# Kernel tuning notes

Measured on AMD Instinct MI355X. Metric: run time of the kernel, lower is better.

## Reference

```python
import jax, jax.numpy as jnp
from jax import lax
import numpy as np

GRID, IMG, BLOCK = 60, 960, 16
BN_EPS = 1e-5


def _conv(x, w, b):
    return lax.conv_general_dilated(x, w, (1, 1), 'SAME', dimension_numbers=('NCHW', 'OIHW', 'NCHW')) + b[None, :, None, None]


def _bn(x, g, b):
    # inference BatchNorm with running_mean=0, running_var=1
    s = g * np.float32(1.0 / np.sqrt(1.0 + BN_EPS))
    return x * s[None, :, None, None] + b[None, :, None, None]


def _mlp(x, w1, b1, w2, b2):
    return jax.nn.relu(x @ w1.T + b1) @ w2.T + b2


def _lstm_layer(x, wih, whh, b):
    # x: [B,T,D]; torch gate order i,f,g,o; zero initial state
    B = x.shape[0]
    H = whh.shape[1]
    pre = jnp.swapaxes(x, 0, 1) @ wih.T + b  # [T,B,4H]

    def step(carry, p):
        h, c = carry
        z = p + h @ whh.T
        i, f, g, o = jnp.split(z, 4, axis=-1)
        c = jax.nn.sigmoid(f) * c + jax.nn.sigmoid(i) * jnp.tanh(g)
        h = jax.nn.sigmoid(o) * jnp.tanh(c)
        return (h, c), h

    z0 = jnp.zeros((B, H), x.dtype)
    (h, c), ys = lax.scan(step, (z0, z0), pre)
    return jnp.swapaxes(ys, 0, 1), h, c


def _forward(motion_vectors, boxes, track_ids, conv1_w, conv1_b, bn1_g, bn1_b, conv2_w, conv2_b, bn2_g, bn2_b, conv3_w, conv3_b, bn3_g, bn3_b, agg_w1, agg_b1, agg_w2, agg_b2, bx_w1, bx_b1, bx_w2, bx_b2, id_table, proj_w, proj_b, empty_slot, l0_wih, l0_whh, l0_b, l1_wih, l1_whh, l1_b, hb_w1, hb_b1, hb_w2, hb_b2, hc_w1, hc_b1, hc_w2, hc_b2, ht_w1, ht_b1, ht_w2, ht_b2):
    B = motion_vectors.shape[0]
    # ---- grid encoder (Conv-BN-ReLU x3) ----
    x = jax.nn.relu(_bn(_conv(motion_vectors, conv1_w, conv1_b), bn1_g, bn1_b))
    x = jax.nn.relu(_bn(_conv(x, conv2_w, conv2_b), bn2_g, bn2_b))
    gf = jax.nn.relu(_bn(_conv(x, conv3_w, conv3_b), bn3_g, bn3_b))  # [B,64,60,60]
    global_feat = gf.mean((-2, -1))  # AdaptiveAvgPool2d(1) -> [B,64]

    # ---- per-box motion statistics (vectorized masked reductions) ----
    bg = jnp.clip(boxes * (IMG / BLOCK), 0.0, GRID - 1e-6)  # grid coords
    ix1 = jnp.floor(bg[..., 0]); iy1 = jnp.floor(bg[..., 1])
    ix2 = jnp.maximum(ix1 + 1.0, jnp.ceil(bg[..., 2]))
    iy2 = jnp.maximum(iy1 + 1.0, jnp.ceil(bg[..., 3]))
    g = jnp.arange(GRID, dtype=bg.dtype)
    mx_ = (g >= ix1[..., None]) & (g < ix2[..., None])  # [B,N,60]
    my_ = (g >= iy1[..., None]) & (g < iy2[..., None])
    mask = my_[..., :, None] & mx_[..., None, :]  # [B,N,60,60]
    m = mask.astype(bg.dtype)
    cnt = m.sum((-2, -1))[..., None]  # [B,N,1], >= 1 by construction
    mv = motion_vectors  # [B,2,60,60]
    s1 = jnp.einsum('bnyx,bcyx->bnc', m, mv)
    s2 = jnp.einsum('bnyx,bcyx->bnc', m, mv * mv)
    mean = s1 / cnt
    var = (s2 - cnt * mean * mean) / jnp.maximum(cnt - 1.0, 1.0)  # unbiased, like torch .std()
    var_safe = jnp.where(cnt > 1.0, jnp.maximum(var, 1e-12), 1.0)
    std = jnp.where(cnt > 1.0, jnp.sqrt(var_safe), 0.0)
    BIG = jnp.asarray(1e9, bg.dtype)
    mn = jnp.min(jnp.where(mask[:, :, None], mv[:, None], BIG), axis=(-2, -1))   # [B,N,2]
    mx = jnp.max(jnp.where(mask[:, :, None], mv[:, None], -BIG), axis=(-2, -1))  # [B,N,2]
    stats = jnp.stack([mean[..., 0], mean[..., 1], std[..., 0], std[..., 1], mn[..., 0], mx[..., 0], mn[..., 1], mx[..., 1]], -1)  # [B,N,8]
    motion_emb = _mlp(stats, agg_w1, agg_b1, agg_w2, agg_b2)  # [B,N,64]

    # ---- slot initialization ----
    box_emb = _mlp(boxes, bx_w1, bx_b1, bx_w2, bx_b2)  # [B,N,64]
    id_emb = id_table[jnp.clip(track_ids, 0, 999)]  # [B,N,32]
    obj = jnp.concatenate([box_emb, id_emb, motion_emb], -1)  # [B,N,160]
    slots = obj @ proj_w.T + proj_b  # [B,300,128]; N == max_slots so no empty slots used

    # ---- 2-layer LSTM over the 300 slots (batch_first, eval -> no dropout) ----
    Ns = slots.shape[1]
    gexp = jnp.broadcast_to(global_feat[:, None, :], (B, Ns, global_feat.shape[-1]))
    lstm_in = jnp.concatenate([slots, gexp], -1)  # [B,300,192]
    y, h0, c0 = _lstm_layer(lstm_in, l0_wih, l0_whh, l0_b)
    y, h1, c1 = _lstm_layer(y, l1_wih, l1_whh, l1_b)  # [B,300,128]

    # ---- RT-DETR style heads ----
    pred_boxes = jax.nn.sigmoid(_mlp(y, hb_w1, hb_b1, hb_w2, hb_b2))  # [B,300,4]
    cls_logits = _mlp(y, hc_w1, hc_b1, hc_w2, hc_b2)  # [B,300,2]
    tid_logits = _mlp(y, ht_w1, ht_b1, ht_w2, ht_b2)  # [B,300,1000]
    h = jnp.stack([h0, h1])
    c = jnp.stack([c0, c1])
    return pred_boxes, cls_logits, tid_logits, h, c


def setup_inputs() -> dict:
    B, N = 32, 300
    key = jax.random.key(0)
    ks = iter(jax.random.split(key, 60))

    def w(*s):
        return jax.random.normal(next(ks), s, jnp.float32) * 0.05

    mv = jax.random.normal(next(ks), (B, 2, GRID, GRID), jnp.float32)
    bb = jax.random.uniform(next(ks), (B, N, 4), jnp.float32)
    boxes = jnp.concatenate([jnp.minimum(bb[..., :2], bb[..., 2:]), jnp.maximum(bb[..., :2], bb[..., 2:])], -1)
    track_ids = jax.random.randint(next(ks), (B, N), 0, 1000)
    return dict(
        motion_vectors=mv, boxes=boxes, track_ids=track_ids,
        conv1_w=w(32, 2, 3, 3), conv1_b=w(32), bn1_g=1.0 + w(32), bn1_b=w(32),
        conv2_w=w(64, 32, 3, 3), conv2_b=w(64), bn2_g=1.0 + w(64), bn2_b=w(64),
        conv3_w=w(64, 64, 3, 3), conv3_b=w(64), bn3_g=1.0 + w(64), bn3_b=w(64),
        agg_w1=w(32, 8), agg_b1=w(32), agg_w2=w(64, 32), agg_b2=w(64),
        bx_w1=w(32, 4), bx_b1=w(32), bx_w2=w(64, 32), bx_b2=w(64),
        id_table=w(1000, 32).at[0].set(0.0),
        proj_w=w(128, 160), proj_b=w(128), empty_slot=w(128),
        l0_wih=w(512, 192), l0_whh=w(512, 128), l0_b=w(512),
        l1_wih=w(512, 128), l1_whh=w(512, 128), l1_b=w(512),
        hb_w1=w(256, 128), hb_b1=w(256), hb_w2=w(4, 256), hb_b2=w(4),
        hc_w1=w(256, 128), hc_b1=w(256), hc_w2=w(2, 256), hc_b2=w(2),
        ht_w1=w(256, 128), ht_b1=w(256), ht_w2=w(1000, 256), ht_b2=w(1000))


def reference(motion_vectors, boxes, track_ids, conv1_w, conv1_b, bn1_g, bn1_b, conv2_w, conv2_b, bn2_g, bn2_b, conv3_w, conv3_b, bn3_g, bn3_b, agg_w1, agg_b1, agg_w2, agg_b2, bx_w1, bx_b1, bx_w2, bx_b2, id_table, proj_w, proj_b, empty_slot, l0_wih, l0_whh, l0_b, l1_wih, l1_whh, l1_b, hb_w1, hb_b1, hb_w2, hb_b2, hc_w1, hc_b1, hc_w2, hc_b2, ht_w1, ht_b1, ht_w2, ht_b2):
    return _forward(motion_vectors, boxes, track_ids, conv1_w, conv1_b, bn1_g, bn1_b, conv2_w, conv2_b, bn2_g, bn2_b, conv3_w, conv3_b, bn3_g, bn3_b, agg_w1, agg_b1, agg_w2, agg_b2, bx_w1, bx_b1, bx_w2, bx_b2, id_table, proj_w, proj_b, empty_slot, l0_wih, l0_whh, l0_b, l1_wih, l1_whh, l1_b, hb_w1, hb_b1, hb_w2, hb_b2, hc_w1, hc_b1, hc_w2, hc_b2, ht_w1, ht_b1, ht_w2, ht_b2)
```

## Files before the change

kernel.cpp:

```cpp
#include <hip/hip_runtime.h>
#include <hip/hip_bf16.h>
#include <math.h>

typedef unsigned short ushort_t;
typedef __attribute__((ext_vector_type(8))) short bf16x8;
typedef __attribute__((ext_vector_type(4))) float f32x4;

#define LOG2E 1.4426950408889634f

__device__ __forceinline__ float sigf(float x) {
  x = fminf(fmaxf(x, -30.f), 30.f);
  return 1.f / (1.f + __expf(-x));
}
__device__ __forceinline__ ushort_t f2bf(float x) {
  unsigned int b = __float_as_uint(x);
  unsigned int lsb = (b >> 16) & 1u;
  b += 0x7fffu + lsb;
  return (ushort_t)(b >> 16);
}
__device__ __forceinline__ float bf2f(ushort_t u) {
  return __uint_as_float(((unsigned int)u) << 16);
}
__device__ __forceinline__ float gsc(int g3) {
  return (g3 == 2) ? (2.f * LOG2E) : LOG2E;
}

#define NPIX 3600
__device__ __forceinline__ int gperm(int rho) {
  return ((rho & 3) << 7) + (rho >> 2);
}

__global__ __launch_bounds__(256) void gvec_kernel(
    const float* __restrict__ wih0, const float* __restrict__ gf,
    float* __restrict__ gvec) {
  int i = blockIdx.x * 256 + threadIdx.x;
  int b = i >> 9, n = i & 511;
  const float* wr = wih0 + gperm(n) * 192 + 128;
  const float* g = gf + b * 64;
  float a = 0.f;
#pragma unroll
  for (int k = 0; k < 64; ++k) a = fmaf(wr[k], g[k], a);
  gvec[i] = a * (1.f / 3600.f) * gsc(n & 3);
}

__global__ __launch_bounds__(256) void front_kernel(
    const float* __restrict__ mv, const float* __restrict__ c1w,
    const float* __restrict__ c1b, const float* __restrict__ bg1,
    const float* __restrict__ bb1, ushort_t* __restrict__ x1out,
    const float* __restrict__ boxes, const int* __restrict__ ids,
    const float* __restrict__ agg_w1, const float* __restrict__ agg_b1,
    const float* __restrict__ agg_w2, const float* __restrict__ agg_b2,
    const float* __restrict__ bx_w1, const float* __restrict__ bx_b1,
    const float* __restrict__ bx_w2, const float* __restrict__ bx_b2,
    const float* __restrict__ id_table, ushort_t* __restrict__ obj_out,
    const float* __restrict__ conv2_w, const float* __restrict__ conv3_w,
    const float* __restrict__ wih0, const float* __restrict__ projW,
    const float* __restrict__ projb, const float* __restrict__ l0_b,
    const float* __restrict__ hbw1, const float* __restrict__ hcw1,
    const float* __restrict__ htw1, const float* __restrict__ htw2,
    const float* __restrict__ hbb1, const float* __restrict__ hcb1,
    const float* __restrict__ htb1, ushort_t* __restrict__ wc2,
    ushort_t* __restrict__ wc3, ushort_t* __restrict__ wAp,
    float* __restrict__ l0bp, ushort_t* __restrict__ whid,
    ushort_t* __restrict__ wt2, float* __restrict__ bhid) {
  if (blockIdx.x < 1989) {
    int i = blockIdx.x * 256 + threadIdx.x;
    if (i < 18432) {
      int oc = i / 288, r = i % 288, kt = r / 32, ic = r % 32;
      wc2[i] = f2bf(conv2_w[((oc * 32 + ic) * 3 + kt / 3) * 3 + kt % 3]);
      return;
    }
    i -= 18432;
    if (i < 36864) {
      int oc = i / 576, r = i % 576, c = r / 288, r2 = r % 288;
      int kt = r2 / 32, icl = r2 % 32, ic = c * 32 + icl;
      wc3[i] = f2bf(conv3_w[((oc * 64 + ic) * 3 + kt / 3) * 3 + kt % 3]);
      return;
    }
    i -= 36864;
    if (i < 98304) {
      int n = i / 192, k = i % 192;
      int src = gperm(n);
      float a = 0.f;
      if (k < 160) {
        const float* wr = wih0 + src * 192;
        for (int j = 0; j < 128; ++j) a = fmaf(wr[j], projW[j * 160 + k], a);
      }
      wAp[i] = f2bf(a * gsc(n & 3));
      return;
    }
    i -= 98304;
    if (i < 512) {
      int src = gperm(i);
      float a = l0_b[src];
      const float* wr = wih0 + src * 192;
      for (int j = 0; j < 128; ++j) a = fmaf(wr[j], projb[j], a);
      l0bp[i] = a * gsc(i & 3);
      return;
    }
    i -= 512;
    if (i < 98304) {
      int row = i >> 7, c = i & 127;
      float v = (row < 256)   ? hbw1[row * 128 + c]
                : (row < 512) ? hcw1[(row - 256) * 128 + c]
                              : htw1[(row - 512) * 128 + c];
      whid[i] = f2bf(v);
      return;
    }
    i -= 98304;
    if (i < 256000) {
      wt2[i] = f2bf(htw2[i]);
      return;
    }
    i -= 256000;
    if (i < 768)
      bhid[i] = (i < 256) ? hbb1[i] : (i < 512) ? hcb1[i - 256] : htb1[i - 512];
    return;
  }
  int bx = blockIdx.x - 1989;
  if (bx < 14400) {
    int idx = bx * 256 + threadIdx.x;
    int x = idx % 60;
    int y = (idx / 60) % 60;
    int oc = (idx / 3600) % 32;
    int b = idx / (3600 * 32);
    float acc = 0.f;
#pragma unroll
    for (int ic = 0; ic < 2; ++ic) {
      const float* src = mv + (b * 2 + ic) * NPIX;
      const float* wp = c1w + (oc * 2 + ic) * 9;
#pragma unroll
      for (int ky = 0; ky < 3; ++ky) {
        int gy = y + ky - 1;
        if (gy < 0 || gy >= 60) continue;
#pragma unroll
        for (int kx = 0; kx < 3; ++kx) {
          int gx = x + kx - 1;
          if (gx < 0 || gx >= 60) continue;
          acc = fmaf(src[gy * 60 + gx], wp[ky * 3 + kx], acc);
        }
      }
    }
    float s = bg1[oc] * rsqrtf(1.f + 1e-5f);
    float v = fmaf(acc, s, fmaf(c1b[oc], s, bb1[oc]));
    x1out[idx] = f2bf(fmaxf(v, 0.f));
    return;
  }
  __shared__ float obj[2][160];
  __shared__ float hm[2][32];
  __shared__ float hbx[2][32];
  __shared__ float stats[2][8];
  __shared__ float boxf[2][4];
  __shared__ float red[2][2][8];
  int h = threadIdx.x >> 7;
  int t = threadIdx.x & 127;
  int blk = (bx - 14400) * 2 + h;
  int b = blk / 300;
  float bx0 = boxes[blk * 4 + 0], by0 = boxes[blk * 4 + 1];
  float bx1 = boxes[blk * 4 + 2], by1 = boxes[blk * 4 + 3];
  const float HI = (float)(60.0 - 1e-6);
  float gx1 = fminf(fmaxf(bx0 * 60.f, 0.f), HI);
  float gy1 = fminf(fmaxf(by0 * 60.f, 0.f), HI);
  float gx2 = fminf(fmaxf(bx1 * 60.f, 0.f), HI);
  float gy2 = fminf(fmaxf(by1 * 60.f, 0.f), HI);
  float fx1 = floorf(gx1), fy1 = floorf(gy1);
  float fx2 = fmaxf(fx1 + 1.f, ceilf(gx2));
  float fy2 = fmaxf(fy1 + 1.f, ceilf(gy2));
  int ix1 = (int)fx1, iy1 = (int)fy1, ix2 = (int)fx2, iy2 = (int)fy2;
  int w = ix2 - ix1, hgt = iy2 - iy1;
  int area = w * hgt;
  float s0 = 0.f, s1 = 0.f, q0 = 0.f, q1 = 0.f;
  float mn0 = 1e9f, mn1 = 1e9f, mx0 = -1e9f, mx1 = -1e9f;
  const float* mv0 = mv + b * 2 * NPIX;
  const float* mv1 = mv0 + NPIX;
  for (int i = t; i < area; i += 128) {
    int r = i / w, cc = i - r * w;
    int yy = iy1 + r, xx = ix1 + cc;
    float v0 = mv0[yy * 60 + xx];
    float v1 = mv1[yy * 60 + xx];
    s0 += v0; q0 += v0 * v0; mn0 = fminf(mn0, v0); mx0 = fmaxf(mx0, v0);
    s1 += v1; q1 += v1 * v1; mn1 = fminf(mn1, v1); mx1 = fmaxf(mx1, v1);
  }
#pragma unroll
  for (int off = 32; off; off >>= 1) {
    s0 += __shfl_down(s0, off); s1 += __shfl_down(s1, off);
    q0 += __shfl_down(q0, off); q1 += __shfl_down(q1, off);
    mn0 = fminf(mn0, __shfl_down(mn0, off));
    mn1 = fminf(mn1, __shfl_down(mn1, off));
    mx0 = fmaxf(mx0, __shfl_down(mx0, off));
    mx1 = fmaxf(mx1, __shfl_down(mx1, off));
  }
  if ((t & 63) == 0) {
    int wv = t >> 6;
    red[h][wv][0] = s0; red[h][wv][1] = s1;
    red[h][wv][2] = q0; red[h][wv][3] = q1;
    red[h][wv][4] = mn0; red[h][wv][5] = mn1;
    red[h][wv][6] = mx0; red[h][wv][7] = mx1;
  }
  __syncthreads();
  if (t == 0) {
    float S0 = red[h][0][0] + red[h][1][0], S1 = red[h][0][1] + red[h][1][1];
    float Q0 = red[h][0][2] + red[h][1][2], Q1 = red[h][0][3] + red[h][1][3];
    float MN0 = fminf(red[h][0][4], red[h][1][4]);
    float MN1 = fminf(red[h][0][5], red[h][1][5]);
    float MX0 = fmaxf(red[h][0][6], red[h][1][6]);
    float MX1 = fmaxf(red[h][0][7], red[h][1][7]);
    float cnt = (float)area;
    float mean0 = S0 / cnt, mean1 = S1 / cnt;
    float var0 = (Q0 - cnt * mean0 * mean0) / fmaxf(cnt - 1.f, 1.f);
    float var1 = (Q1 - cnt * mean1 * mean1) / fmaxf(cnt - 1.f, 1.f);
    float sd0 = (cnt > 1.f) ? sqrtf(fmaxf(var0, 1e-12f)) : 0.f;
    float sd1 = (cnt > 1.f) ? sqrtf(fmaxf(var1, 1e-12f)) : 0.f;
    stats[h][0] = mean0; stats[h][1] = mean1; stats[h][2] = sd0;
    stats[h][3] = sd1; stats[h][4] = MN0; stats[h][5] = MX0;
    stats[h][6] = MN1; stats[h][7] = MX1;
    boxf[h][0] = bx0; boxf[h][1] = by0; boxf[h][2] = bx1; boxf[h][3] = by1;
  }
  __syncthreads();
  if (t < 32) {
    float a = agg_b1[t];
#pragma unroll
    for (int k = 0; k < 8; ++k) a = fmaf(stats[h][k], agg_w1[t * 8 + k], a);
    hm[h][t] = fmaxf(a, 0.f);
  } else if (t < 64) {
    int j = t - 32;
    float a = bx_b1[j];
#pragma unroll
    for (int k = 0; k < 4; ++k) a = fmaf(boxf[h][k], bx_w1[j * 4 + k], a);
    hbx[h][j] = fmaxf(a, 0.f);
  }
  __syncthreads();
  if (t < 64) {
    float a = bx_b2[t];
#pragma unroll
    for (int k = 0; k < 32; ++k) a = fmaf(hbx[h][k], bx_w2[t * 32 + k], a);
    obj[h][t] = a;
  } else {
    int j = t - 64;
    float a = agg_b2[j];
#pragma unroll
    for (int k = 0; k < 32; ++k) a = fmaf(hm[h][k], agg_w2[j * 32 + k], a);
    obj[h][96 + j] = a;
  }
  if (t < 32) {
    int id = ids[blk];
    id = min(max(id, 0), 999);
    obj[h][64 + t] = id_table[id * 32 + t];
  }
  __syncthreads();
  obj_out[(size_t)blk * 192 + t] = f2bf(obj[h][t]);
  if (t < 32) {
    obj_out[(size_t)blk * 192 + 128 + t] = f2bf(obj[h][128 + t]);
    obj_out[(size_t)blk * 192 + 160 + t] = 0;
  }
}

template <int CIN, bool POOL>
__global__ __launch_bounds__(256) void conv_mfma_kernel(
    const ushort_t* __restrict__ in, const ushort_t* __restrict__ wc,
    const float* __restrict__ cb, const float* __restrict__ bg,
    const float* __restrict__ bb, ushort_t* __restrict__ out,
    float* __restrict__ gf) {
  constexpr int NCHUNK = CIN / 32;
  __shared__ ushort_t in_lds[18 * 18 * 40];
  int tid = threadIdx.x;
  int wv = tid >> 6, lane = tid & 63;
  int col = lane & 15, kg = lane >> 4;
  int b = blockIdx.y, tile = blockIdx.x;
  int tq = tile >> 2, tr = tile & 3;
  int ty0 = tq * 16 - (tq == 3 ? 4 : 0);
  int tx0 = tr * 16 - (tr == 3 ? 4 : 0);
  int oc = wv * 16 + col;

  bf16x8 bw[NCHUNK * 9];
#pragma unroll
  for (int c = 0; c < NCHUNK; ++c)
#pragma unroll
    for (int kt = 0; kt < 9; ++kt)
      bw[c * 9 + kt] = *(const bf16x8*)(wc + oc * (NCHUNK * 288) + c * 288 +
                                        kt * 32 + kg * 8);

  f32x4 acc[16];
#pragma unroll
  for (int m = 0; m < 16; ++m) acc[m] = (f32x4){0.f, 0.f, 0.f, 0.f};

  for (int c = 0; c < NCHUNK; ++c) {
    if (c) __syncthreads();
    for (int i = tid; i < 18 * 18 * 32; i += 256) {
      int ic = i / 324, rem = i % 324;
      int yy = rem / 18, xx = rem % 18;
      int gy = ty0 + yy - 1, gx = tx0 + xx - 1;
      ushort_t v = 0;
      if (gy >= 0 && gy < 60 && gx >= 0 && gx < 60)
        v = in[((size_t)(b * CIN + c * 32 + ic) * 60 + gy) * 60 + gx];
      in_lds[(yy * 18 + xx) * 40 + ic] = v;
    }
    __syncthreads();
#pragma unroll
    for (int kt = 0; kt < 9; ++kt) {
      int ky = kt / 3, kx = kt % 3;
#pragma unroll
      for (int m = 0; m < 16; ++m) {
        bf16x8 af =
            *(const bf16x8*)(&in_lds[((m + ky) * 18 + col + kx) * 40 + kg * 8]);
        acc[m] = __builtin_amdgcn_mfma_f32_16x16x32_bf16(af, bw[c * 9 + kt],
                                                         acc[m], 0, 0, 0);
      }
    }
  }
  float s = bg[oc] * rsqrtf(1.f + 1e-5f);
  float bias = fmaf(cb[oc], s, bb[oc]);
  float pool = 0.f;
#pragma unroll
  for (int m = 0; m < 16; ++m) {
    float vv[4];
#pragma unroll
    for (int r = 0; r < 4; ++r) vv[r] = fmaxf(fmaf(acc[m][r], s, bias), 0.f);
    if (POOL) {
      bool ymask = (tq != 3) || (m >= 4);
#pragma unroll
      for (int r = 0; r < 4; ++r) {
        int px = kg * 4 + r;
        bool xmask = (tr != 3) || (px >= 4);
        if (ymask && xmask) pool += vv[r];
      }
    } else {
      ushort_t st[4];
#pragma unroll
      for (int r = 0; r < 4; ++r) st[r] = f2bf(vv[r]);
      int yy = ty0 + m, xx = tx0 + kg * 4;
      *(uint2*)(&out[((size_t)(b * 64 + oc) * 60 + yy) * 60 + xx]) =
          *(uint2*)st;
    }
  }
  if (POOL) {
    pool += __shfl_xor(pool, 16);
    pool += __shfl_xor(pool, 32);
    if (lane < 16) atomicAdd(&gf[b * 64 + oc], pool);
  }
}

template <int ACT, bool OBF16, bool GVEC>
__global__ __launch_bounds__(256) void gemm_bf16w_kernel(
    const ushort_t* __restrict__ A, int lda, const ushort_t* __restrict__ W,
    const float* __restrict__ bias, void* __restrict__ C, int ldc, int M,
    int N, int K, const float* __restrict__ gvec) {
  __shared__ ushort_t As[128 * 64];
  __shared__ ushort_t Ws[64 * 64];
  int tid = threadIdx.x;
  int wv = tid >> 6, lane = tid & 63;
  int col = lane & 15, kg = lane >> 4;
  int wm = wv >> 1, wn = wv & 1;
  int m0 = blockIdx.x * 128, n0 = blockIdx.y * 64;
  f32x4 acc[4][2];
#pragma unroll
  for (int i = 0; i < 4; ++i)
#pragma unroll
    for (int j = 0; j < 2; ++j) acc[i][j] = (f32x4){0.f, 0.f, 0.f, 0.f};

  int nk = K >> 6;
  for (int kc = 0; kc < nk; ++kc) {
    if (kc) __syncthreads();
#pragma unroll
    for (int q = 0; q < 4; ++q) {
      int idx = q * 256 + tid;
      int row = idx >> 3, ch = idx & 7;
      uint4 v =
          *(const uint4*)(A + (size_t)(m0 + row) * lda + kc * 64 + ch * 8);
      *(uint4*)(&As[row * 64 + ((ch * 8) ^ ((row & 7) << 3))]) = v;
    }
#pragma unroll
    for (int q = 0; q < 2; ++q) {
      int idx = q * 256 + tid;
      int row = idx >> 3, ch = idx & 7;
      int n = n0 + row;
      uint4 v = make_uint4(0, 0, 0, 0);
      if (n < N) v = *(const uint4*)(W + (size_t)n * K + kc * 64 + ch * 8);
      *(uint4*)(&Ws[row * 64 + ((ch * 8) ^ ((row & 7) << 3))]) = v;
    }
    __syncthreads();
#pragma unroll
    for (int ks = 0; ks < 2; ++ks) {
      bf16x8 bfr[2], afr[4];
#pragma unroll
      for (int ni = 0; ni < 2; ++ni) {
        int row = wn * 32 + ni * 16 + col;
        bfr[ni] = *(const bf16x8*)(
            &Ws[row * 64 + ((ks * 32 + kg * 8) ^ ((row & 7) << 3))]);
      }
#pragma unroll
      for (int mi = 0; mi < 4; ++mi) {
        int row = wm * 64 + mi * 16 + col;
        afr[mi] = *(const bf16x8*)(
            &As[row * 64 + ((ks * 32 + kg * 8) ^ ((row & 7) << 3))]);
      }
#pragma unroll
      for (int mi = 0; mi < 4; ++mi)
#pragma unroll
        for (int ni = 0; ni < 2; ++ni)
          acc[mi][ni] = __builtin_amdgcn_mfma_f32_16x16x32_bf16(
              afr[mi], bfr[ni], acc[mi][ni], 0, 0, 0);
    }
  }
#pragma unroll
  for (int ni = 0; ni < 2; ++ni) {
    int n = n0 + wn * 32 + ni * 16 + col;
    float bn = (n < N) ? bias[n] : 0.f;
#pragma unroll
    for (int mi = 0; mi < 4; ++mi) {
      int mbase = m0 + wm * 64 + mi * 16 + kg * 4;
#pragma unroll
      for (int r = 0; r < 4; ++r) {
        float v = acc[mi][ni][r] + bn;
        if (GVEC) v += gvec[((mbase + r) / 300) * 512 + n];
        if (ACT == 1) v = fmaxf(v, 0.f);
        if (n < N) {
          if (OBF16)
            ((ushort_t*)C)[(size_t)(mbase + r) * ldc + n] = f2bf(v);
          else
            ((float*)C)[(size_t)(mbase + r) * ldc + n] = v;
        }
      }
    }
  }
}

__global__ __launch_bounds__(256) void head_small_kernel(
    const ushort_t* __restrict__ hid, const float* __restrict__ wb2,
    const float* __restrict__ bb2, const float* __restrict__ wc2,
    const float* __restrict__ bc2, float* __restrict__ outB,
    float* __restrict__ outC) {
  int idx = blockIdx.x * 256 + threadIdx.x;
  int row = idx / 6, j = idx % 6;
  const ushort_t* h = hid + (size_t)row * 768 + (j < 4 ? 0 : 256);
  const float* wrow = (j < 4) ? wb2 + j * 256 : wc2 + (j - 4) * 256;
  float acc = (j < 4) ? bb2[j] : bc2[j - 4];
  for (int k = 0; k < 256; k += 8) {
    uint4 hv = *(const uint4*)(h + k);
    unsigned int ww[4] = {hv.x, hv.y, hv.z, hv.w};
#pragma unroll
    for (int q = 0; q < 4; ++q) {
      acc = fmaf(bf2f((ushort_t)(ww[q] & 0xffff)), wrow[k + 2 * q], acc);
      acc = fmaf(bf2f((ushort_t)(ww[q] >> 16)), wrow[k + 2 * q + 1], acc);
    }
  }
  float v = (j < 4) ? sigf(acc) : acc;
  if (j < 4) outB[row * 4 + j] = v;
  else outC[row * 2 + (j - 4)] = v;
}

#define LSTM_BAR() asm volatile("s_waitcnt lgkmcnt(0)\n\ts_barrier" ::: "memory")

__global__ __launch_bounds__(512) void lstm_fused_kernel(
    const float* __restrict__ pre0,
    const float* __restrict__ whh0,
    const float* __restrict__ wih1,
    const float* __restrict__ whh1,
    const float* __restrict__ b1,
    float* __restrict__ pre1,
    ushort_t* __restrict__ y0,
    ushort_t* __restrict__ y1,
    float* __restrict__ outH, float* __restrict__ outC,
    unsigned int* __restrict__ flags)
{
  __shared__ ushort_t h_lds[2][4][160];
  int tid = threadIdx.x;
  int w = tid >> 6, lane = tid & 63;
  int col = lane & 15, kg = lane >> 4;
  int bat = col & 3, q = col >> 2;
  int cell = (4 * w + q) * 4 + kg;
  float wsc = gsc(col & 3);

  if (blockIdx.x < 8) {
    int g = blockIdx.x;
    int b0 = g * 4;
    unsigned int* flagp = &flags[g * 32];
    for (int i = tid; i < 2 * 4 * 160; i += 512) ((ushort_t*)h_lds)[i] = 0;
    bf16x8 aW0[4][4];
#pragma unroll
    for (int j = 0; j < 4; ++j) {
      int rho = (4 * w + j) * 16 + col;
      int src = gperm(rho);
#pragma unroll
      for (int kt = 0; kt < 4; ++kt) {
        const float* s1 = whh0 + src * 128 + kt * 32 + kg * 8;
        bf16x8 f1;
#pragma unroll
        for (int qq = 0; qq < 8; ++qq) f1[qq] = (short)f2bf(s1[qq] * wsc);
        aW0[j][kt] = f1;
      }
    }
    const float* pg = pre0 + (size_t)(b0 + bat) * 300 * 512 + 4 * cell;
    ushort_t* yg0 = y0 + ((size_t)(b0 + bat) * 300) * 128 + cell;
    float c = 0.f, hout = 0.f;
    f32x4 p0v = *(const f32x4*)(pg);
    f32x4 p1v = *(const f32x4*)(pg + 512);
    __syncthreads();

    for (int s = 0; s < 300; ++s) {
      const ushort_t* hb = h_lds[s & 1][bat];
      bf16x8 bfr[4];
#pragma unroll
      for (int kt = 0; kt < 4; ++kt)
        bfr[kt] = *(const bf16x8*)(hb + kt * 32 + kg * 8);
      f32x4 a0 = {0.f, 0.f, 0.f, 0.f}, a1 = a0, a2 = a0, a3 = a0;
#pragma unroll
      for (int kt = 0; kt < 4; ++kt) {
        a0 = __builtin_amdgcn_mfma_f32_16x16x32_bf16(aW0[0][kt], bfr[kt], a0, 0, 0, 0);
        a1 = __builtin_amdgcn_mfma_f32_16x16x32_bf16(aW0[1][kt], bfr[kt], a1, 0, 0, 0);
        a2 = __builtin_amdgcn_mfma_f32_16x16x32_bf16(aW0[2][kt], bfr[kt], a2, 0, 0, 0);
        a3 = __builtin_amdgcn_mfma_f32_16x16x32_bf16(aW0[3][kt], bfr[kt], a3, 0, 0, 0);
      }
      f32x4 z = a0;
      if (q == 1) z = a1;
      if (q == 2) z = a2;
      if (q == 3) z = a3;
      {
        float zi = z[0] + p0v[0];
        float zf = z[1] + p0v[1];
        float zg = z[2] + p0v[2];
        float zo = z[3] + p0v[3];
        float vi = __builtin_amdgcn_rcpf(1.f + __builtin_amdgcn_exp2f(-zi));
        float vf = __builtin_amdgcn_rcpf(1.f + __builtin_amdgcn_exp2f(-zf));
        float vg = 1.f - 2.f * __builtin_amdgcn_rcpf(
                              __builtin_amdgcn_exp2f(zg) + 1.f);
        float vo = __builtin_amdgcn_rcpf(1.f + __builtin_amdgcn_exp2f(-zo));
        c = vf * c + vi * vg;
        hout = vo * (1.f - 2.f * __builtin_amdgcn_rcpf(
                             __builtin_amdgcn_exp2f(2.f * LOG2E * c) + 1.f));
        ushort_t hv = f2bf(hout);
        h_lds[(s + 1) & 1][bat][cell] = hv;
        __builtin_nontemporal_store(hv, yg0 + (size_t)s * 128);
        p0v = p1v;
        int sn = (s + 2 < 300) ? s + 2 : 299;
        p1v = *(const f32x4*)(pg + (size_t)sn * 512);
      }
      asm volatile("s_waitcnt vmcnt(6)" ::: "memory");
      LSTM_BAR();
      if (tid == 0 && s >= 3)
        __hip_atomic_store(flagp, (unsigned int)(s - 3), __ATOMIC_RELAXED,
                           __HIP_MEMORY_SCOPE_AGENT);
    }
    asm volatile("s_waitcnt vmcnt(0)" ::: "memory");
    __syncthreads();
    if (tid == 0)
      __hip_atomic_store(flagp, 300u, __ATOMIC_RELAXED,
                         __HIP_MEMORY_SCOPE_AGENT);
    outH[(b0 + bat) * 128 + cell] = hout;
    outC[(b0 + bat) * 128 + cell] = c;
  } else if (blockIdx.x < 16) {
    int g = blockIdx.x - 8;
    int b0 = g * 4;
    unsigned int* flagp = &flags[g * 32 + 16];
    for (int i = tid; i < 2 * 4 * 160; i += 512) ((ushort_t*)h_lds)[i] = 0;
    bf16x8 aW[4][4];
#pragma unroll
    for (int j = 0; j < 4; ++j) {
      int rho = (4 * w + j) * 16 + col;
      int src = gperm(rho);
#pragma unroll
      for (int kt = 0; kt < 4; ++kt) {
        const float* s1 = whh1 + src * 128 + kt * 32 + kg * 8;
        bf16x8 f1;
#pragma unroll
        for (int qq = 0; qq < 8; ++qq) f1[qq] = (short)f2bf(s1[qq] * wsc);
        aW[j][kt] = f1;
      }
    }
    float bi = b1[cell] * LOG2E, bff = b1[128 + cell] * LOG2E;
    float bgg = b1[256 + cell] * (2.f * LOG2E), boo = b1[384 + cell] * LOG2E;
    const float* pg = pre1 + (size_t)(b0 + bat) * 300 * 512 + 4 * cell;
    ushort_t* yg = y1 + (size_t)(b0 + bat) * 300 * 128 + cell;
    float c = 0.f, hout = 0.f;
    unsigned int fc = 0;
    f32x4 p0v, p1v;
    do {
      fc = __hip_atomic_load(flagp, __ATOMIC_RELAXED,
                             __HIP_MEMORY_SCOPE_AGENT);
      if (fc < 1) __builtin_amdgcn_s_sleep(2);
    } while (fc < 1);
    asm volatile("" ::: "memory");
    p0v = __builtin_nontemporal_load((const f32x4*)(pg));
    while (fc < 2) {
      fc = __hip_atomic_load(flagp, __ATOMIC_RELAXED,
                             __HIP_MEMORY_SCOPE_AGENT);
      if (fc < 2) __builtin_amdgcn_s_sleep(2);
    }
    asm volatile("" ::: "memory");
    p1v = __builtin_nontemporal_load((const f32x4*)(pg + 512));
    __syncthreads();

    for (int t = 0; t < 300; ++t) {
      unsigned int fcn = __hip_atomic_load(flagp, __ATOMIC_RELAXED,
                                           __HIP_MEMORY_SCOPE_AGENT);
      const ushort_t* hb = h_lds[t & 1][bat];
      bf16x8 bfr[4];
#pragma unroll
      for (int kt = 0; kt < 4; ++kt)
        bfr[kt] = *(const bf16x8*)(hb + kt * 32 + kg * 8);
      f32x4 a0 = {0.f, 0.f, 0.f, 0.f}, a1 = a0, a2 = a0, a3 = a0;
#pragma unroll
      for (int kt = 0; kt < 4; ++kt) {
        a0 = __builtin_amdgcn_mfma_f32_16x16x32_bf16(aW[0][kt], bfr[kt], a0, 0, 0, 0);
        a1 = __builtin_amdgcn_mfma_f32_16x16x32_bf16(aW[1][kt], bfr[kt], a1, 0, 0, 0);
        a2 = __builtin_amdgcn_mfma_f32_16x16x32_bf16(aW[2][kt], bfr[kt], a2, 0, 0, 0);
        a3 = __builtin_amdgcn_mfma_f32_16x16x32_bf16(aW[3][kt], bfr[kt], a3, 0, 0, 0);
      }
      f32x4 z = a0;
      if (q == 1) z = a1;
      if (q == 2) z = a2;
      if (q == 3) z = a3;
      {
        float zi = z[0] + p0v[0] + bi;
        float zf = z[1] + p0v[1] + bff;
        float zg = z[2] + p0v[2] + bgg;
        float zo = z[3] + p0v[3] + boo;
        float vi = __builtin_amdgcn_rcpf(1.f + __builtin_amdgcn_exp2f(-zi));
        float vf = __builtin_amdgcn_rcpf(1.f + __builtin_amdgcn_exp2f(-zf));
        float vg = 1.f - 2.f * __builtin_amdgcn_rcpf(
                              __builtin_amdgcn_exp2f(zg) + 1.f);
        float vo = __builtin_amdgcn_rcpf(1.f + __builtin_amdgcn_exp2f(-zo));
        c = vf * c + vi * vg;
        hout = vo * (1.f - 2.f * __builtin_amdgcn_rcpf(
                             __builtin_amdgcn_exp2f(2.f * LOG2E * c) + 1.f));
        ushort_t hv = f2bf(hout);
        h_lds[(t + 1) & 1][bat][cell] = hv;
        yg[(size_t)t * 128] = hv;
        p0v = p1v;
        if (t + 2 < 300) {
          unsigned int need = (unsigned int)(t + 3);
          if (fcn > fc) fc = fcn;
          if (fc < need) {
            do {
              fc = __hip_atomic_load(flagp, __ATOMIC_RELAXED,
                                     __HIP_MEMORY_SCOPE_AGENT);
              if (fc < need) __builtin_amdgcn_s_sleep(2);
            } while (fc < need);
            asm volatile("" ::: "memory");
          }
          p1v = __builtin_nontemporal_load(
              (const f32x4*)(pg + (size_t)(t + 2) * 512));
        }
      }
      LSTM_BAR();
    }
    outH[4096 + (b0 + bat) * 128 + cell] = hout;
    outC[4096 + (b0 + bat) * 128 + cell] = c;
  } else {
    int g = blockIdx.x - 16;
    int b0 = g * 4;
    unsigned int* flag0 = &flags[g * 32];
    unsigned int* flag1 = &flags[g * 32 + 16];
    bf16x8 aU[4][4];
#pragma unroll
    for (int j = 0; j < 4; ++j) {
      int rho = (4 * w + j) * 16 + col;
      int src = gperm(rho);
#pragma unroll
      for (int kt = 0; kt < 4; ++kt) {
        const float* s2 = wih1 + src * 128 + kt * 32 + kg * 8;
        bf16x8 f2;
#pragma unroll
        for (int qq = 0; qq < 8; ++qq) f2[qq] = (short)f2bf(s2[qq] * wsc);
        aU[j][kt] = f2;
      }
    }
    int bb = col & 3;
    int ts = col >> 2;
    const ushort_t* yb = y0 + ((size_t)(b0 + bb) * 300) * 128 + kg * 8;
    unsigned int fc = 0;
    for (int t0 = 0; t0 < 300; t0 += 12) {
      unsigned int need = (unsigned int)(t0 + 11);
      while (fc < need) {
        fc = __hip_atomic_load(flag0, __ATOMIC_RELAXED,
                               __HIP_MEMORY_SCOPE_AGENT);
        if (fc < need) __builtin_amdgcn_s_sleep(2);
      }
      asm volatile("" ::: "memory");
      f32x4 acc[4][3];
#pragma unroll
      for (int j = 0; j < 4; ++j)
#pragma unroll
        for (int ct = 0; ct < 3; ++ct) acc[j][ct] = (f32x4){0.f, 0.f, 0.f, 0.f};
#pragma unroll
      for (int ct = 0; ct < 3; ++ct) {
        int t = t0 + ct * 4 + ts;
        bf16x8 bfr[4];
#pragma unroll
        for (int kt = 0; kt < 4; ++kt)
          bfr[kt] = __builtin_nontemporal_load(
              (const bf16x8*)(yb + (size_t)t * 128 + kt * 32));
#pragma unroll
        for (int kt = 0; kt < 4; ++kt) {
          acc[0][ct] = __builtin_amdgcn_mfma_f32_16x16x32_bf16(aU[0][kt], bfr[kt], acc[0][ct], 0, 0, 0);
          acc[1][ct] = __builtin_amdgcn_mfma_f32_16x16x32_bf16(aU[1][kt], bfr[kt], acc[1][ct], 0, 0, 0);
          acc[2][ct] = __builtin_amdgcn_mfma_f32_16x16x32_bf16(aU[2][kt], bfr[kt], acc[2][ct], 0, 0, 0);
          acc[3][ct] = __builtin_amdgcn_mfma_f32_16x16x32_bf16(aU[3][kt], bfr[kt], acc[3][ct], 0, 0, 0);
        }
      }
#pragma unroll
      for (int ct = 0; ct < 3; ++ct) {
        int t = t0 + ct * 4 + ts;
        float* pd = pre1 + ((size_t)(b0 + bb) * 300 + t) * 512 + kg * 4;
#pragma unroll
        for (int j = 0; j < 4; ++j)
          __builtin_nontemporal_store(acc[j][ct],
                                      (f32x4*)(pd + (4 * w + j) * 16));
      }
      asm volatile("s_waitcnt vmcnt(0)" ::: "memory");
      __syncthreads();
      if (tid == 0)
        __hip_atomic_store(flag1, (unsigned int)(t0 + 12), __ATOMIC_RELAXED,
                           __HIP_MEMORY_SCOPE_AGENT);
    }
  }
}

extern "C" void kernel_launch(void* const* d_in, const int* in_sizes, int n_in,
                              void* d_out, int out_size, void* d_ws,
                              size_t ws_size, hipStream_t stream) {
  const float* mv = (const float*)d_in[0];
  const float* boxes = (const float*)d_in[1];
  const int* track_ids = (const int*)d_in[2];
  const float* conv1_w = (const float*)d_in[3];
  const float* conv1_b = (const float*)d_in[4];
  const float* bn1_g = (const float*)d_in[5];
  const float* bn1_b = (const float*)d_in[6];
  const float* conv2_w = (const float*)d_in[7];
  const float* conv2_b = (const float*)d_in[8];
  const float* bn2_g = (const float*)d_in[9];
  const float* bn2_b = (const float*)d_in[10];
  const float* conv3_w = (const float*)d_in[11];
  const float* conv3_b = (const float*)d_in[12];
  const float* bn3_g = (const float*)d_in[13];
  const float* bn3_b = (const float*)d_in[14];
  const float* agg_w1 = (const float*)d_in[15];
  const float* agg_b1 = (const float*)d_in[16];
  const float* agg_w2 = (const float*)d_in[17];
  const float* agg_b2 = (const float*)d_in[18];
  const float* bx_w1 = (const float*)d_in[19];
  const float* bx_b1 = (const float*)d_in[20];
  const float* bx_w2 = (const float*)d_in[21];
  const float* bx_b2 = (const float*)d_in[22];
  const float* id_table = (const float*)d_in[23];
  const float* proj_w = (const float*)d_in[24];
  const float* proj_b = (const float*)d_in[25];
  const float* l0_wih = (const float*)d_in[27];
  const float* l0_whh = (const float*)d_in[28];
  const float* l0_b = (const float*)d_in[29];
  const float* l1_wih = (const float*)d_in[30];
  const float* l1_whh = (const float*)d_in[31];
  const float* l1_b = (const float*)d_in[32];
  const float* hb_w1 = (const float*)d_in[33];
  const float* hb_b1 = (const float*)d_in[34];
  const float* hb_w2 = (const float*)d_in[35];
  const float* hb_b2 = (const float*)d_in[36];
  const float* hc_w1 = (const float*)d_in[37];
  const float* hc_b1 = (const float*)d_in[38];
  const float* hc_w2 = (const float*)d_in[39];
  const float* hc_b2 = (const float*)d_in[40];
  const float* ht_w1 = (const float*)d_in[41];
  const float* ht_b1 = (const float*)d_in[42];
  const float* ht_w2 = (const float*)d_in[43];
  const float* ht_b2 = (const float*)d_in[44];

  char* wsb = (char*)d_ws;
  ushort_t* x1u = (ushort_t*)(wsb + 0);
  ushort_t* x2u = (ushort_t*)(wsb + 7372800);
  float* pre0 = (float*)(wsb + 0);
  ushort_t* hid = (ushort_t*)(wsb + 0);
  ushort_t* y0g = (ushort_t*)(wsb + 19660800);
  float* gf = (float*)(wsb + 22118400);
  ushort_t* obj = (ushort_t*)(wsb + 22126592);
  float* pre1 = (float*)(wsb + 25812992);
  ushort_t* y1b = (ushort_t*)(wsb + 45473792);
  unsigned int* flags = (unsigned int*)(wsb + 47931392);
  ushort_t* wAp = (ushort_t*)(wsb + 47932416);
  ushort_t* whid = (ushort_t*)(wsb + 48129024);
  ushort_t* wt2 = (ushort_t*)(wsb + 48325632);
  float* bhid = (float*)(wsb + 48837632);
  float* l0bp = (float*)(wsb + 48840704);
  float* gvec = (float*)(wsb + 48842752);
  ushort_t* wc2 = (ushort_t*)(wsb + 48908288);
  ushort_t* wc3 = (ushort_t*)(wsb + 48945152);

  float* outB = (float*)d_out;
  float* outC = outB + 38400;
  float* outT = outB + 57600;
  float* outH = outB + 9657600;
  float* outCc = outB + 9665792;

  hipMemsetAsync(gf, 0, 2048 * sizeof(float), stream);
  hipMemsetAsync(flags, 0, 1024, stream);

  front_kernel<<<21189, 256, 0, stream>>>(
      mv, conv1_w, conv1_b, bn1_g, bn1_b, x1u, boxes, track_ids, agg_w1,
      agg_b1, agg_w2, agg_b2, bx_w1, bx_b1, bx_w2, bx_b2, id_table, obj,
      conv2_w, conv3_w, l0_wih, proj_w, proj_b, l0_b, hb_w1, hc_w1, ht_w1,
      ht_w2, hb_b1, hc_b1, ht_b1, wc2, wc3, wAp, l0bp, whid, wt2, bhid);
  conv_mfma_kernel<32, false><<<dim3(16, 32), 256, 0, stream>>>(
      x1u, wc2, conv2_b, bn2_g, bn2_b, x2u, nullptr);
  conv_mfma_kernel<64, true><<<dim3(16, 32), 256, 0, stream>>>(
      x2u, wc3, conv3_b, bn3_g, bn3_b, nullptr, gf);
  gvec_kernel<<<64, 256, 0, stream>>>(l0_wih, gf, gvec);
  gemm_bf16w_kernel<0, false, true><<<dim3(75, 8), 256, 0, stream>>>(
      obj, 192, wAp, l0bp, pre0, 512, 9600, 512, 192, gvec);
  lstm_fused_kernel<<<24, 512, 0, stream>>>(pre0, l0_whh, l1_wih, l1_whh,
                                            l1_b, pre1, y0g, y1b, outH, outCc,
                                            flags);
  gemm_bf16w_kernel<1, true, false><<<dim3(75, 12), 256, 0, stream>>>(
      y1b, 128, whid, bhid, hid, 768, 9600, 768, 128, nullptr);
  head_small_kernel<<<225, 256, 0, stream>>>(hid, hb_w2, hb_b2, hc_w2, hc_b2,
                                             outB, outC);
  gemm_bf16w_kernel<0, false, false><<<dim3(75, 16), 256, 0, stream>>>(
      hid + 512, 768, wt2, ht_b2, outT, 1000, 9600, 1000, 256, nullptr);
}
```

Baseline: 543.4 us.

## Fuse output heads into LSTM kernel as flag-gated consumer blocks overlapping recurrence

The three head kernels (hidden MLP GEMM, box/class small heads, track GEMM) move into extra blocks of the fused LSTM kernel. The layer-1 blocks publish a progress flag every 30 timesteps, and 80 new blocks each wait for their 30-step chunk before computing that chunk's head outputs. Head work can then overlap the serial LSTM recurrence instead of running after it. In exchange, pre0's workspace is reused as the hidden buffer, the layer-1 loop gains periodic full waits and barriers, and correctness depends on enough blocks being co-resident so the spinning consumers do not starve the producers.

```diff
diff --git a/kernel.cpp b/kernel.cpp
--- a/kernel.cpp
+++ b/kernel.cpp
@@ -425,34 +425,10 @@
   }
 }
 
-__global__ __launch_bounds__(256) void head_small_kernel(
-    const ushort_t* __restrict__ hid, const float* __restrict__ wb2,
-    const float* __restrict__ bb2, const float* __restrict__ wc2,
-    const float* __restrict__ bc2, float* __restrict__ outB,
-    float* __restrict__ outC) {
-  int idx = blockIdx.x * 256 + threadIdx.x;
-  int row = idx / 6, j = idx % 6;
-  const ushort_t* h = hid + (size_t)row * 768 + (j < 4 ? 0 : 256);
-  const float* wrow = (j < 4) ? wb2 + j * 256 : wc2 + (j - 4) * 256;
-  float acc = (j < 4) ? bb2[j] : bc2[j - 4];
-  for (int k = 0; k < 256; k += 8) {
-    uint4 hv = *(const uint4*)(h + k);
-    unsigned int ww[4] = {hv.x, hv.y, hv.z, hv.w};
-#pragma unroll
-    for (int q = 0; q < 4; ++q) {
-      acc = fmaf(bf2f((ushort_t)(ww[q] & 0xffff)), wrow[k + 2 * q], acc);
-      acc = fmaf(bf2f((ushort_t)(ww[q] >> 16)), wrow[k + 2 * q + 1], acc);
-    }
-  }
-  float v = (j < 4) ? sigf(acc) : acc;
-  if (j < 4) outB[row * 4 + j] = v;
-  else outC[row * 2 + (j - 4)] = v;
-}
-
 #define LSTM_BAR() asm volatile("s_waitcnt lgkmcnt(0)\n\ts_barrier" ::: "memory")
 
 __global__ __launch_bounds__(512) void lstm_fused_kernel(
-    const float* __restrict__ pre0,
+    const float* pre0,
     const float* __restrict__ whh0,
     const float* __restrict__ wih1,
     const float* __restrict__ whh1,
@@ -461,21 +437,28 @@
     ushort_t* __restrict__ y0,
     ushort_t* __restrict__ y1,
     float* __restrict__ outH, float* __restrict__ outC,
-    unsigned int* __restrict__ flags)
-{
-  __shared__ ushort_t h_lds[2][4][160];
+    unsigned int* __restrict__ flags,
+    ushort_t* hid16,
+    const ushort_t* __restrict__ whid, const ushort_t* __restrict__ wt2,
+    const float* __restrict__ bhid, const float* __restrict__ hbw2,
+    const float* __restrict__ hbb2, const float* __restrict__ hcw2,
+    const float* __restrict__ hcb2, const float* __restrict__ htb2,
+    float* __restrict__ outB, float* __restrict__ outCls,
+    float* __restrict__ outT) {
+  __shared__ ushort_t smem[30720];
   int tid = threadIdx.x;
   int w = tid >> 6, lane = tid & 63;
   int col = lane & 15, kg = lane >> 4;
   int bat = col & 3, q = col >> 2;
   int cell = (4 * w + q) * 4 + kg;
   float wsc = gsc(col & 3);
+  ushort_t (*h_lds)[4][160] = (ushort_t(*)[4][160])smem;
 
   if (blockIdx.x < 8) {
     int g = blockIdx.x;
     int b0 = g * 4;
     unsigned int* flagp = &flags[g * 32];
-    for (int i = tid; i < 2 * 4 * 160; i += 512) ((ushort_t*)h_lds)[i] = 0;
+    for (int i = tid; i < 2 * 4 * 160; i += 512) smem[i] = 0;
     bf16x8 aW0[4][4];
 #pragma unroll
     for (int j = 0; j < 4; ++j) {
@@ -552,7 +535,8 @@
     int g = blockIdx.x - 8;
     int b0 = g * 4;
     unsigned int* flagp = &flags[g * 32 + 16];
-    for (int i = tid; i < 2 * 4 * 160; i += 512) ((ushort_t*)h_lds)[i] = 0;
+    unsigned int* flagy1 = &flags[g * 32 + 17];
+    for (int i = tid; i < 2 * 4 * 160; i += 512) smem[i] = 0;
     bf16x8 aW[4][4];
 #pragma unroll
     for (int j = 0; j < 4; ++j) {
@@ -642,11 +626,18 @@
               (const f32x4*)(pg + (size_t)(t + 2) * 512));
         }
       }
+      if ((t % 30) == 29) {
+        asm volatile("s_waitcnt vmcnt(0)" ::: "memory");
+        __syncthreads();
+        if (tid == 0)
+          __hip_atomic_store(flagy1, (unsigned int)(t + 1), __ATOMIC_RELAXED,
+                             __HIP_MEMORY_SCOPE_AGENT);
+      }
       LSTM_BAR();
     }
     outH[4096 + (b0 + bat) * 128 + cell] = hout;
     outC[4096 + (b0 + bat) * 128 + cell] = c;
-  } else {
+  } else if (blockIdx.x < 24) {
     int g = blockIdx.x - 16;
     int b0 = g * 4;
     unsigned int* flag0 = &flags[g * 32];
@@ -712,6 +703,137 @@
       if (tid == 0)
         __hip_atomic_store(flag1, (unsigned int)(t0 + 12), __ATOMIC_RELAXED,
                            __HIP_MEMORY_SCOPE_AGENT);
+    }
+  } else {
+    int idx2 = blockIdx.x - 24;
+    int g = idx2 & 7, ck = idx2 >> 3;
+    int b0 = g * 4, t0 = ck * 30;
+    unsigned int* flagy = &flags[g * 32 + 17];
+    unsigned int need = (unsigned int)(t0 + 30);
+    unsigned int fc = 0;
+    while (fc < need) {
+      fc = __hip_atomic_load(flagy, __ATOMIC_RELAXED,
+                             __HIP_MEMORY_SCOPE_AGENT);
+      if (fc < need) __builtin_amdgcn_s_sleep(8);
+    }
+    asm volatile("" ::: "memory");
+    int wm = w >> 2, wn = w & 3;
+    int Rt[4][4];
+    bool Vt[4][4];
+#pragma unroll
+    for (int mi = 0; mi < 4; ++mi)
+#pragma unroll
+      for (int r = 0; r < 4; ++r) {
+        int m = wm * 64 + mi * 16 + kg * 4 + r;
+        Vt[mi][r] = (m < 120);
+        int mm = (m < 120) ? m : 119;
+        Rt[mi][r] = (b0 + mm / 30) * 300 + t0 + mm % 30;
+      }
+    ushort_t* As = smem;
+    ushort_t* Wt = smem + 16384;
+    for (int i = tid; i < 2048; i += 512) {
+      int r = i >> 4, ch = i & 15;
+      uint4 v = make_uint4(0, 0, 0, 0);
+      if (r < 120) {
+        int R = (b0 + r / 30) * 300 + t0 + r % 30;
+        v = *(const uint4*)(y1 + (size_t)R * 128 + ch * 8);
+      }
+      *(uint4*)(&As[r * 128 + ((ch * 8) ^ ((r & 7) << 3))]) = v;
+    }
+    __syncthreads();
+    for (int nt = 0; nt < 12; ++nt) {
+      if (nt) __syncthreads();
+      for (int i = tid; i < 1024; i += 512) {
+        int r = i >> 4, ch = i & 15;
+        uint4 v = *(const uint4*)(whid + (size_t)(nt * 64 + r) * 128 + ch * 8);
+        *(uint4*)(&Wt[r * 128 + ((ch * 8) ^ ((r & 7) << 3))]) = v;
+      }
+      __syncthreads();
+      f32x4 acc[4];
+#pragma unroll
+      for (int mi = 0; mi < 4; ++mi) acc[mi] = (f32x4){0.f, 0.f, 0.f, 0.f};
+      int rl = wn * 16 + col;
+#pragma unroll
+      for (int ks = 0; ks < 4; ++ks) {
+        bf16x8 bfr = *(const bf16x8*)(
+            &Wt[rl * 128 + ((ks * 32 + kg * 8) ^ ((rl & 7) << 3))]);
+#pragma unroll
+        for (int mi = 0; mi < 4; ++mi) {
+          int rm = wm * 64 + mi * 16 + col;
+          bf16x8 afr = *(const bf16x8*)(
+              &As[rm * 128 + ((ks * 32 + kg * 8) ^ ((rm & 7) << 3))]);
+          acc[mi] = __builtin_amdgcn_mfma_f32_16x16x32_bf16(afr, bfr, acc[mi],
+                                                            0, 0, 0);
+        }
+      }
+      int n = nt * 64 + wn * 16 + col;
+      float bn = bhid[n];
+#pragma unroll
+      for (int mi = 0; mi < 4; ++mi)
+#pragma unroll
+        for (int r = 0; r < 4; ++r)
+          if (Vt[mi][r]) {
+            float v = fmaxf(acc[mi][r] + bn, 0.f);
+            hid16[(size_t)Rt[mi][r] * 1024 + n] = f2bf(v);
+          }
+    }
+    asm volatile("s_waitcnt vmcnt(0)" ::: "memory");
+    __syncthreads();
+    for (int o = tid; o < 720; o += 512) {
+      int m = o / 6, j = o % 6;
+      int R = (b0 + m / 30) * 300 + t0 + m % 30;
+      const ushort_t* hsrc = hid16 + (size_t)R * 1024 + (j < 4 ? 0 : 256);
+      const float* wrow = (j < 4) ? hbw2 + j * 256 : hcw2 + (j - 4) * 256;
+      float a = (j < 4) ? hbb2[j] : hcb2[j - 4];
+      for (int k = 0; k < 256; k += 8) {
+        uint4 hv = *(const uint4*)(hsrc + k);
+        unsigned int wq[4] = {hv.x, hv.y, hv.z, hv.w};
+#pragma unroll
+        for (int qq = 0; qq < 4; ++qq) {
+          a = fmaf(bf2f((ushort_t)(wq[qq] & 0xffff)), wrow[k + 2 * qq], a);
+          a = fmaf(bf2f((ushort_t)(wq[qq] >> 16)), wrow[k + 2 * qq + 1], a);
+        }
+      }
+      if (j < 4) outB[R * 4 + j] = sigf(a);
+      else outCls[R * 2 + (j - 4)] = a;
+    }
+    __syncthreads();
+    ushort_t* As2 = smem;
+    for (int i = tid; i < 3840; i += 512) {
+      int r = i >> 5, ch = i & 31;
+      int R = (b0 + r / 30) * 300 + t0 + r % 30;
+      uint4 v = *(const uint4*)(hid16 + (size_t)R * 1024 + 512 + ch * 8);
+      *(uint4*)(&As2[r * 256 + ((ch * 8) ^ ((r & 7) << 3))]) = v;
+    }
+    __syncthreads();
+    for (int nt = 0; nt < 16; ++nt) {
+      f32x4 acc[4];
+#pragma unroll
+      for (int mi = 0; mi < 4; ++mi) acc[mi] = (f32x4){0.f, 0.f, 0.f, 0.f};
+      int n = nt * 64 + wn * 16 + col;
+      int nc = (n < 1000) ? n : 999;
+#pragma unroll
+      for (int ks = 0; ks < 8; ++ks) {
+        bf16x8 bfr =
+            *(const bf16x8*)(wt2 + (size_t)nc * 256 + ks * 32 + kg * 8);
+#pragma unroll
+        for (int mi = 0; mi < 4; ++mi) {
+          int rm = wm * 64 + mi * 16 + col;
+          int rc = (rm < 120) ? rm : 119;
+          bf16x8 afr = *(const bf16x8*)(
+              &As2[rc * 256 + ((ks * 32 + kg * 8) ^ ((rc & 7) << 3))]);
+          acc[mi] = __builtin_amdgcn_mfma_f32_16x16x32_bf16(afr, bfr, acc[mi],
+                                                            0, 0, 0);
+        }
+      }
+      float bn = htb2[nc];
+      bool nok = (n < 1000);
+#pragma unroll
+      for (int mi = 0; mi < 4; ++mi)
+#pragma unroll
+        for (int r = 0; r < 4; ++r)
+          if (Vt[mi][r] && nok)
+            outT[(size_t)Rt[mi][r] * 1000 + n] = acc[mi][r] + bn;
     }
   }
 }
@@ -768,7 +890,6 @@
   ushort_t* x1u = (ushort_t*)(wsb + 0);
   ushort_t* x2u = (ushort_t*)(wsb + 7372800);
   float* pre0 = (float*)(wsb + 0);
-  ushort_t* hid = (ushort_t*)(wsb + 0);
   ushort_t* y0g = (ushort_t*)(wsb + 19660800);
   float* gf = (float*)(wsb + 22118400);
   ushort_t* obj = (ushort_t*)(wsb + 22126592);
@@ -805,13 +926,8 @@
   gvec_kernel<<<64, 256, 0, stream>>>(l0_wih, gf, gvec);
   gemm_bf16w_kernel<0, false, true><<<dim3(75, 8), 256, 0, stream>>>(
       obj, 192, wAp, l0bp, pre0, 512, 9600, 512, 192, gvec);
-  lstm_fused_kernel<<<24, 512, 0, stream>>>(pre0, l0_whh, l1_wih, l1_whh,
-                                            l1_b, pre1, y0g, y1b, outH, outCc,
-                                            flags);
-  gemm_bf16w_kernel<1, true, false><<<dim3(75, 12), 256, 0, stream>>>(
-      y1b, 128, whid, bhid, hid, 768, 9600, 768, 128, nullptr);
-  head_small_kernel<<<225, 256, 0, stream>>>(hid, hb_w2, hb_b2, hc_w2, hc_b2,
-                                             outB, outC);
-  gemm_bf16w_kernel<0, false, false><<<dim3(75, 16), 256, 0, stream>>>(
-      hid + 512, 768, wt2, ht_b2, outT, 1000, 9600, 1000, 256, nullptr);
-}
+  lstm_fused_kernel<<<104, 512, 0, stream>>>(
+      pre0, l0_whh, l1_wih, l1_whh, l1_b, pre1, y0g, y1b, outH, outCc, flags,
+      (ushort_t*)pre0, whid, wt2, bhid, hb_w2, hb_b2, hc_w2, hc_b2, ht_b2,
+      outB, outC, outT);
+}
```

New measurement: 628.6 us. 15.7% more time.
